# Kernel optimization log

Hardware: AMD Instinct MI355X
Metric: run time of the kernel (lower is better)

The kernel has to match this reference:

```python
import jax, jax.numpy as jnp
import numpy as np

D_MODEL = 1024
N_HEADS = 16
D_FF = 4096
EPS = 1e-5


def setup_inputs() -> dict:
    key = jax.random.key(0)
    ks = jax.random.split(key, 16)
    B, S, D, F = 2, 2048, D_MODEL, D_FF
    s_d = 1.0 / np.sqrt(D)
    s_f = 1.0 / np.sqrt(F)
    return {
        "x": jax.random.normal(ks[0], (B, S, D), dtype=jnp.float32),
        "pad_mask": jnp.ones((B, S), dtype=jnp.int32),
        "ln1_g": jnp.ones((D,), jnp.float32), "ln1_b": jnp.zeros((D,), jnp.float32),
        "ln2_g": jnp.ones((D,), jnp.float32), "ln2_b": jnp.zeros((D,), jnp.float32),
        # weights stored [in, out] (equivalent to torch Linear weight.T)
        "wq": jax.random.normal(ks[1], (D, D), jnp.float32) * s_d,
        "bq": jnp.zeros((D,), jnp.float32),
        "wk": jax.random.normal(ks[2], (D, D), jnp.float32) * s_d,
        "bk": jnp.zeros((D,), jnp.float32),
        "wv": jax.random.normal(ks[3], (D, D), jnp.float32) * s_d,
        "bv": jnp.zeros((D,), jnp.float32),
        "wo": jax.random.normal(ks[4], (D, D), jnp.float32) * s_d,
        "bo": jnp.zeros((D,), jnp.float32),
        "w1": jax.random.normal(ks[5], (D, F), jnp.float32) * s_d,
        "b1": jnp.zeros((F,), jnp.float32),
        "w2": jax.random.normal(ks[6], (F, D), jnp.float32) * s_f,
        "b2": jnp.zeros((D,), jnp.float32),
    }


def _layernorm(x, g, b):
    mu = jnp.mean(x, axis=-1, keepdims=True)
    var = jnp.mean(jnp.square(x - mu), axis=-1, keepdims=True)
    return (x - mu) * jax.lax.rsqrt(var + EPS) * g + b


def reference(x, pad_mask, ln1_g, ln1_b, ln2_g, ln2_b,
              wq, bq, wk, bk, wv, bv, wo, bo, w1, b1, w2, b2):
    B, S, D = x.shape
    H = N_HEADS
    dk = D // H

    # mask: causal [1,1,S,S] * pad [B,1,1,S]
    causal = jnp.tril(jnp.ones((S, S), dtype=jnp.int32))[None, None]
    mask = pad_mask[:, None, None, :] * causal  # [B,1,S,S]

    h = _layernorm(x, ln1_g, ln1_b)
    q = (h @ wq + bq).reshape(B, S, H, dk).transpose(0, 2, 1, 3)
    k = (h @ wk + bk).reshape(B, S, H, dk).transpose(0, 2, 1, 3)
    v = (h @ wv + bv).reshape(B, S, H, dk).transpose(0, 2, 1, 3)

    scores = jnp.einsum('bhqd,bhkd->bhqk', q, k) / np.sqrt(dk)
    scores = jnp.where(mask == 0, -jnp.inf, scores)
    attn = jax.nn.softmax(scores, axis=-1)
    ctx = jnp.einsum('bhqk,bhkd->bhqd', attn, v)
    ctx = ctx.transpose(0, 2, 1, 3).reshape(B, S, D)
    x = x + ctx @ wo + bo

    h2 = _layernorm(x, ln2_g, ln2_b)
    ff = jax.nn.gelu(h2 @ w1 + b1, approximate=False) @ w2 + b2
    return x + ff
```

## Files before the change

kernel.cpp:

```cpp
#include <hip/hip_runtime.h>
#include <math.h>


typedef unsigned short bfu;
typedef unsigned short u16x4 __attribute__((ext_vector_type(4)));
typedef unsigned short u16x8 __attribute__((ext_vector_type(8)));
typedef __bf16         bf16x8 __attribute__((ext_vector_type(8)));
typedef float          f32x4 __attribute__((ext_vector_type(4)));

#define SEQ   2048
#define NTOK  4096
#define DM    1024
#define DKH   64

static __device__ __forceinline__ float bfu2f(bfu u) {
  return __uint_as_float(((unsigned)u) << 16);
}
static __device__ __forceinline__ bfu f2bfu(float f) {
  unsigned u = __float_as_uint(f);
  u += 0x7FFFu + ((u >> 16) & 1u);
  return (bfu)(u >> 16);
}
static __device__ __forceinline__ float ldF(const void* p, size_t i, bool isbf) {
  return isbf ? bfu2f(((const bfu*)p)[i]) : ((const float*)p)[i];
}
static __device__ __forceinline__ bool dt_isbf(const void* dt) {
  return *(const unsigned*)dt == 0x3F803F80u;
}
static __device__ __forceinline__ void g2l16(const void* g, void* l) {
  __builtin_amdgcn_global_load_lds((const __attribute__((address_space(1))) void*)g,
                                   (__attribute__((address_space(3))) void*)l,
                                   16, 0, 0);
}

static __device__ __forceinline__ void tr_tile(const void* in, bfu* out,
                                               int R, int C, int gx, int gy,
                                               bool isbf, bfu t[64][65]) {
  const int tx = threadIdx.x & 63, ty = threadIdx.x >> 6;
#pragma unroll
  for (int i = 0; i < 16; ++i) {
    int rr = i * 4 + ty;
    size_t idx = (size_t)(gy + rr) * C + gx + tx;
    t[rr][tx] = isbf ? ((const bfu*)in)[idx] : f2bfu(((const float*)in)[idx]);
  }
  __syncthreads();
#pragma unroll
  for (int i = 0; i < 16; ++i) {
    int cc = i * 4 + ty;
    out[(size_t)(gx + cc) * R + gy + tx] = t[tx][cc];
  }
}

__global__ __launch_bounds__(256) void prep_k(
    const void* ln1g, const void* ln1b, const void* ln2g, const void* ln2b,
    const void* bq, const void* bk, const void* bv, const void* bo,
    const void* b1, const void* b2,
    const void* wq, const void* wk, const void* wv, const void* wo,
    const void* w1, const void* w2,
    bfu* __restrict__ vecs, bfu* __restrict__ wqkvT, bfu* __restrict__ woT,
    bfu* __restrict__ w1T, bfu* __restrict__ w2T) {
  __shared__ bfu t[64][65];
  const bool isbf = dt_isbf(ln1g);
  const int bid = blockIdx.x, tid = threadIdx.x;
  if (bid < 52) {
    const void* src; int segStart, segDst;
    if      (bid < 4)  { src = ln1g; segStart = 0;  segDst = 0; }
    else if (bid < 8)  { src = ln1b; segStart = 4;  segDst = 1024; }
    else if (bid < 12) { src = ln2g; segStart = 8;  segDst = 2048; }
    else if (bid < 16) { src = ln2b; segStart = 12; segDst = 3072; }
    else if (bid < 20) { src = bq;   segStart = 16; segDst = 4096; }
    else if (bid < 24) { src = bk;   segStart = 20; segDst = 5120; }
    else if (bid < 28) { src = bv;   segStart = 24; segDst = 6144; }
    else if (bid < 32) { src = bo;   segStart = 28; segDst = 7168; }
    else if (bid < 48) { src = b1;   segStart = 32; segDst = 8192; }
    else               { src = b2;   segStart = 48; segDst = 12288; }
    const int off = (bid - segStart) * 256 + tid;
    vecs[segDst + off] = isbf ? ((const bfu*)src)[off]
                              : f2bfu(((const float*)src)[off]);
    return;
  }
  const void* in; bfu* out; int R, C, gx, gy;
  const int j = bid - 52;
  if (j < 1024) {
    const int mat = j >> 8, rem = j & 255;
    in  = (mat == 0) ? wq : (mat == 1) ? wk : (mat == 2) ? wv : wo;
    out = (mat == 0) ? wqkvT : (mat == 1) ? wqkvT + 1048576
        : (mat == 2) ? wqkvT + 2097152 : woT;
    R = 1024; C = 1024; gx = (rem & 15) * 64; gy = (rem >> 4) * 64;
  } else if (j < 2048) {
    const int rem = j - 1024;
    in = w1; out = w1T; R = 1024; C = 4096;
    gx = (rem & 63) * 64; gy = (rem >> 6) * 64;
  } else {
    const int rem = j - 2048;
    in = w2; out = w2T; R = 4096; C = 1024;
    gx = (rem & 15) * 64; gy = (rem >> 4) * 64;
  }
  tr_tile(in, out, R, C, gx, gy, isbf, t);
}

__global__ __launch_bounds__(256) void trw2_k(const void* __restrict__ w2,
                                              bfu* __restrict__ out,
                                              const void* __restrict__ dt) {
  __shared__ bfu t[64][65];
  const bool isbf = dt_isbf(dt);
  const int rem = blockIdx.x;
  tr_tile(w2, out, 4096, 1024, (rem & 15) * 64, (rem >> 4) * 64, isbf, t);
}

template <bool RAW>
__global__ __launch_bounds__(256) void ln_k(const void* __restrict__ xin,
                                            const bfu* __restrict__ g,
                                            const bfu* __restrict__ bb,
                                            bfu* __restrict__ y,
                                            const void* __restrict__ dt) {
  const int t = threadIdx.x;
  const size_t base = (size_t)blockIdx.x * DM;
  const int c0 = t * 4;
  float v[4];
  bool isbf = true;
  if constexpr (RAW) isbf = dt_isbf(dt);
  if (!RAW || isbf) {
    u16x4 u = *(const u16x4*)((const bfu*)xin + base + c0);
#pragma unroll
    for (int i = 0; i < 4; ++i) v[i] = bfu2f(u[i]);
  } else {
    float4 f = *(const float4*)((const float*)xin + base + c0);
    v[0] = f.x; v[1] = f.y; v[2] = f.z; v[3] = f.w;
  }
  float s1 = v[0] + v[1] + v[2] + v[3];
  float s2 = v[0]*v[0] + v[1]*v[1] + v[2]*v[2] + v[3]*v[3];
#pragma unroll
  for (int o = 32; o; o >>= 1) {
    s1 += __shfl_xor(s1, o);
    s2 += __shfl_xor(s2, o);
  }
  __shared__ float r1[4], r2[4];
  const int wid = t >> 6, lane = t & 63;
  if (lane == 0) { r1[wid] = s1; r2[wid] = s2; }
  __syncthreads();
  s1 = r1[0] + r1[1] + r1[2] + r1[3];
  s2 = r2[0] + r2[1] + r2[2] + r2[3];
  const float mu = s1 * (1.0f / DM);
  const float var = s2 * (1.0f / DM) - mu * mu;
  const float rs = rsqrtf(var + 1e-5f);
  u16x4 gv = *(const u16x4*)&g[c0];
  u16x4 bv = *(const u16x4*)&bb[c0];
  u16x4 ov;
#pragma unroll
  for (int i = 0; i < 4; ++i)
    ov[i] = f2bfu((v[i] - mu) * rs * bfu2f(gv[i]) + bfu2f(bv[i]));
  *(u16x4*)&y[base + c0] = ov;
}

template <int EPI>
__global__ __launch_bounds__(256) void gemm_bt(const bfu* __restrict__ A,
                                               const bfu* __restrict__ Bt,
                                               const bfu* __restrict__ bias,
                                               const void* __restrict__ res,
                                               void* __restrict__ C,
                                               int M, int N, int K,
                                               const void* __restrict__ dt) {
  __shared__ __align__(16) bfu Asm[128 * 32];
  __shared__ __align__(16) bfu Bsm[128 * 32];
  const bool isbf = dt_isbf(dt);
  const int tid = threadIdx.x;
  const int m0 = blockIdx.y * 128, n0 = blockIdx.x * 128;
  const int wid = tid >> 6, lane = tid & 63;
  const int wm = (wid >> 1) * 64, wn = (wid & 1) * 64;
  const int quad = lane >> 4, l16 = lane & 15;

  f32x4 acc[4][4] = {};

  const int c0 = tid, c1 = tid + 256;
  const bfu* agp0 = A + (size_t)(m0 + (c0 >> 2)) * K + (c0 & 3) * 8;
  const bfu* agp1 = A + (size_t)(m0 + (c1 >> 2)) * K + (c1 & 3) * 8;
  const bfu* bgp0 = Bt + (size_t)(n0 + (c0 >> 2)) * K + (c0 & 3) * 8;
  const bfu* bgp1 = Bt + (size_t)(n0 + (c1 >> 2)) * K + (c1 & 3) * 8;
  bfu* al0 = Asm + c0 * 8;
  bfu* al1 = Asm + c1 * 8;
  bfu* bl0 = Bsm + c0 * 8;
  bfu* bl1 = Bsm + c1 * 8;

  for (int k0 = 0; k0 < K; k0 += 32) {
    g2l16(agp0 + k0, al0);
    g2l16(agp1 + k0, al1);
    g2l16(bgp0 + k0, bl0);
    g2l16(bgp1 + k0, bl1);
    __syncthreads();

    u16x8 af[4], bfr[4];
#pragma unroll
    for (int i = 0; i < 4; ++i)
      af[i] = *(const u16x8*)&Asm[(wm + i * 16 + l16) * 32 + quad * 8];
#pragma unroll
    for (int i = 0; i < 4; ++i)
      bfr[i] = *(const u16x8*)&Bsm[(wn + i * 16 + l16) * 32 + quad * 8];
#pragma unroll
    for (int mi = 0; mi < 4; ++mi)
#pragma unroll
      for (int ni = 0; ni < 4; ++ni)
        acc[mi][ni] = __builtin_amdgcn_mfma_f32_16x16x32_bf16(
            __builtin_bit_cast(bf16x8, af[mi]),
            __builtin_bit_cast(bf16x8, bfr[ni]), acc[mi][ni], 0, 0, 0);
    __syncthreads();
  }

#pragma unroll
  for (int mi = 0; mi < 4; ++mi) {
#pragma unroll
    for (int ni = 0; ni < 4; ++ni) {
      const int col = n0 + wn + ni * 16 + l16;
      const float bvv = bfu2f(bias[col]);
#pragma unroll
      for (int r = 0; r < 4; ++r) {
        const int row = m0 + wm + mi * 16 + quad * 4 + r;
        const size_t idx = (size_t)row * N + col;
        float v = acc[mi][ni][r] + bvv;
        if constexpr (EPI == 1) {
          v = 0.5f * v * (1.0f + erff(v * 0.70710678118f));
          ((bfu*)C)[idx] = f2bfu(v);
        } else if constexpr (EPI == 2) {
          v += ldF(res, idx, isbf);
          ((bfu*)C)[idx] = f2bfu(v);
        } else if constexpr (EPI == 3) {
          v += bfu2f(((const bfu*)res)[idx]);
          if (isbf) ((bfu*)C)[idx] = f2bfu(v);
          else      ((float*)C)[idx] = v;
        } else {
          ((bfu*)C)[idx] = f2bfu(v);
        }
      }
    }
  }
}

template <int EPI>
__global__ __launch_bounds__(256) void gemm32_bt(const bfu* __restrict__ A,
                                                 const bfu* __restrict__ Bt,
                                                 const bfu* __restrict__ bias,
                                                 const void* __restrict__ res,
                                                 void* __restrict__ C,
                                                 int M, int N, int K,
                                                 const void* __restrict__ dt) {
  __shared__ __align__(16) bfu Asm[2 * 32 * 32];
  __shared__ __align__(16) bfu Bsm[2 * 128 * 32];
  const bool isbf = dt_isbf(dt);
  const int tid = threadIdx.x;
  const int m0 = blockIdx.y * 32, n0 = blockIdx.x * 128;
  const int wid = tid >> 6, lane = tid & 63;
  const int wn = wid * 32;
  const int quad = lane >> 4, l16 = lane & 15;

  f32x4 acc[2][2] = {};

  const int pA = tid >> 7, rA = (tid >> 2) & 31, qA = tid & 3;
  const bfu* agp = A + (size_t)(m0 + rA) * K + pA * 32 + qA * 8;
  bfu* aldst = Asm + tid * 8;
  const bfu* bgp[4]; bfu* bldst[4];
#pragma unroll
  for (int s = 0; s < 4; ++s) {
    const int c = tid + s * 256;
    const int pB = c >> 9, rB = (c >> 2) & 127, qB = c & 3;
    bgp[s] = Bt + (size_t)(n0 + rB) * K + pB * 32 + qB * 8;
    bldst[s] = Bsm + c * 8;
  }

  for (int k0 = 0; k0 < K; k0 += 64) {
    g2l16(agp + k0, aldst);
#pragma unroll
    for (int s = 0; s < 4; ++s) g2l16(bgp[s] + k0, bldst[s]);
    __syncthreads();

    u16x8 af[2][2], bfr[2][2];
#pragma unroll
    for (int kt = 0; kt < 2; ++kt) {
#pragma unroll
      for (int mi = 0; mi < 2; ++mi)
        af[mi][kt] = *(const u16x8*)&Asm[kt * 1024 + (mi * 16 + l16) * 32 + quad * 8];
#pragma unroll
      for (int ni = 0; ni < 2; ++ni)
        bfr[ni][kt] = *(const u16x8*)&Bsm[kt * 4096 + (wn + ni * 16 + l16) * 32 + quad * 8];
    }
#pragma unroll
    for (int kt = 0; kt < 2; ++kt)
#pragma unroll
      for (int mi = 0; mi < 2; ++mi)
#pragma unroll
        for (int ni = 0; ni < 2; ++ni)
          acc[mi][ni] = __builtin_amdgcn_mfma_f32_16x16x32_bf16(
              __builtin_bit_cast(bf16x8, af[mi][kt]),
              __builtin_bit_cast(bf16x8, bfr[ni][kt]), acc[mi][ni], 0, 0, 0);
    __syncthreads();
  }

#pragma unroll
  for (int mi = 0; mi < 2; ++mi) {
#pragma unroll
    for (int ni = 0; ni < 2; ++ni) {
      const int col = n0 + wn + ni * 16 + l16;
      const float bvv = bfu2f(bias[col]);
#pragma unroll
      for (int r = 0; r < 4; ++r) {
        const int row = m0 + mi * 16 + quad * 4 + r;
        const size_t idx = (size_t)row * N + col;
        float v = acc[mi][ni][r] + bvv;
        if constexpr (EPI == 1) {
          v = 0.5f * v * (1.0f + erff(v * 0.70710678118f));
          ((bfu*)C)[idx] = f2bfu(v);
        } else if constexpr (EPI == 2) {
          v += ldF(res, idx, isbf);
          ((bfu*)C)[idx] = f2bfu(v);
        } else if constexpr (EPI == 3) {
          v += bfu2f(((const bfu*)res)[idx]);
          if (isbf) ((bfu*)C)[idx] = f2bfu(v);
          else      ((float*)C)[idx] = v;
        } else {
          ((bfu*)C)[idx] = f2bfu(v);
        }
      }
    }
  }
}

#define NEG_BIG (-1e30f)
#define KSTR 72

__global__ __launch_bounds__(256) void attn_flash(const bfu* __restrict__ qkv,
                                                  const int* __restrict__ pad,
                                                  bfu* __restrict__ ctx) {
  __shared__ __align__(16) bfu Kb[64 * KSTR];
  __shared__ __align__(16) bfu VT[64 * KSTR];
  __shared__ __align__(16) bfu Pb[4][16 * KSTR];

  const int tid = threadIdx.x;
  const int wid = tid >> 6, lane = tid & 63;
  const int quad = lane >> 4, l16 = lane & 15;
  const int bh = blockIdx.x;
  const int b = bh >> 4, h = bh & 15;
  const int yq = blockIdx.y;
  const int qt = (yq < 8) ? yq : (yq < 16) ? 23 - yq
               : (yq < 24) ? yq : 55 - yq;
  const int q0 = qt * 64;

  const bfu* qptr = qkv + (size_t)(b * SEQ + q0 + wid * 16 + l16) * 3072 + h * 64 + quad * 8;
  u16x8 qfr[2];
#pragma unroll
  for (int kt = 0; kt < 2; ++kt) {
    u16x8 qr = *(const u16x8*)(qptr + kt * 32);
#pragma unroll
    for (int j = 0; j < 8; ++j) qr[j] = f2bfu(bfu2f(qr[j]) * 0.125f);
    qfr[kt] = qr;
  }

  f32x4 Ofr[4] = {};
  float mrow[4], lrow[4];
#pragma unroll
  for (int r = 0; r < 4; ++r) { mrow[r] = NEG_BIG; lrow[r] = 0.0f; }

  const bfu* kvbase = qkv + (size_t)(b * SEQ) * 3072 + h * 64;
  const int* pb = pad + b * SEQ;
  const int qrow_base = q0 + wid * 16 + quad * 4;

  const int kkey0 = tid >> 3,          kpc0 = tid & 7;
  const int kkey1 = (tid + 256) >> 3,  kpc1 = (tid + 256) & 7;
  const int vkey = tid & 63, dblk = tid >> 6;

  u16x8 kreg0, kreg1, vreg0, vreg1;
  kreg0 = *(const u16x8*)(kvbase + (size_t)kkey0 * 3072 + 1024 + kpc0 * 8);
  kreg1 = *(const u16x8*)(kvbase + (size_t)kkey1 * 3072 + 1024 + kpc1 * 8);
  vreg0 = *(const u16x8*)(kvbase + (size_t)vkey * 3072 + 2048 + dblk * 16);
  vreg1 = *(const u16x8*)(kvbase + (size_t)vkey * 3072 + 2048 + dblk * 16 + 8);

  const int ntiles = qt + 1;
  for (int t = 0; t < ntiles; ++t) {
    const int k0 = t * 64;
    __syncthreads();

    *(u16x8*)&Kb[kkey0 * KSTR + kpc0 * 8] = kreg0;
    *(u16x8*)&Kb[kkey1 * KSTR + kpc1 * 8] = kreg1;
#pragma unroll
    for (int j = 0; j < 8; ++j) VT[(dblk * 16 + j) * KSTR + vkey] = vreg0[j];
#pragma unroll
    for (int j = 0; j < 8; ++j) VT[(dblk * 16 + 8 + j) * KSTR + vkey] = vreg1[j];
    __syncthreads();

    if (t + 1 < ntiles) {
      const int kn = k0 + 64;
      kreg0 = *(const u16x8*)(kvbase + (size_t)(kn + kkey0) * 3072 + 1024 + kpc0 * 8);
      kreg1 = *(const u16x8*)(kvbase + (size_t)(kn + kkey1) * 3072 + 1024 + kpc1 * 8);
      vreg0 = *(const u16x8*)(kvbase + (size_t)(kn + vkey) * 3072 + 2048 + dblk * 16);
      vreg1 = *(const u16x8*)(kvbase + (size_t)(kn + vkey) * 3072 + 2048 + dblk * 16 + 8);
    }

    f32x4 S[4] = {};
#pragma unroll
    for (int nt = 0; nt < 4; ++nt)
#pragma unroll
      for (int kt = 0; kt < 2; ++kt) {
        u16x8 bf = *(const u16x8*)&Kb[(nt * 16 + l16) * KSTR + kt * 32 + quad * 8];
        S[nt] = __builtin_amdgcn_mfma_f32_16x16x32_bf16(
            __builtin_bit_cast(bf16x8, qfr[kt]),
            __builtin_bit_cast(bf16x8, bf), S[nt], 0, 0, 0);
      }

    const bool edge = (t == qt);
    float p[4][4];
    float cmax[4] = {NEG_BIG, NEG_BIG, NEG_BIG, NEG_BIG};
#pragma unroll
    for (int nt = 0; nt < 4; ++nt) {
      const int key = k0 + nt * 16 + l16;
      const bool ok = (pb[key] != 0);
#pragma unroll
      for (int r = 0; r < 4; ++r) {
        float s = (ok && (!edge || key <= qrow_base + r)) ? S[nt][r] : NEG_BIG;
        p[nt][r] = s;
        cmax[r] = fmaxf(cmax[r], s);
      }
    }
#pragma unroll
    for (int off = 1; off < 16; off <<= 1)
#pragma unroll
      for (int r = 0; r < 4; ++r)
        cmax[r] = fmaxf(cmax[r], __shfl_xor(cmax[r], off));
    float alpha[4];
#pragma unroll
    for (int r = 0; r < 4; ++r) {
      const float mn = fmaxf(mrow[r], cmax[r]);
      alpha[r] = __expf(mrow[r] - mn);
      mrow[r] = mn;
    }
    float psum[4] = {0, 0, 0, 0};
#pragma unroll
    for (int nt = 0; nt < 4; ++nt)
#pragma unroll
      for (int r = 0; r < 4; ++r) {
        p[nt][r] = __expf(p[nt][r] - mrow[r]);
        psum[r] += p[nt][r];
      }
#pragma unroll
    for (int off = 1; off < 16; off <<= 1)
#pragma unroll
      for (int r = 0; r < 4; ++r) psum[r] += __shfl_xor(psum[r], off);
#pragma unroll
    for (int r = 0; r < 4; ++r) lrow[r] = lrow[r] * alpha[r] + psum[r];
#pragma unroll
    for (int n = 0; n < 4; ++n)
#pragma unroll
      for (int r = 0; r < 4; ++r) Ofr[n][r] *= alpha[r];

#pragma unroll
    for (int nt = 0; nt < 4; ++nt)
#pragma unroll
      for (int r = 0; r < 4; ++r)
        Pb[wid][(quad * 4 + r) * KSTR + nt * 16 + l16] = f2bfu(p[nt][r]);

#pragma unroll
    for (int at = 0; at < 2; ++at) {
      u16x8 af = *(const u16x8*)&Pb[wid][l16 * KSTR + at * 32 + quad * 8];
#pragma unroll
      for (int n = 0; n < 4; ++n) {
        u16x8 bf = *(const u16x8*)&VT[(n * 16 + l16) * KSTR + at * 32 + quad * 8];
        Ofr[n] = __builtin_amdgcn_mfma_f32_16x16x32_bf16(
            __builtin_bit_cast(bf16x8, af),
            __builtin_bit_cast(bf16x8, bf), Ofr[n], 0, 0, 0);
      }
    }
  }

  float inv[4];
#pragma unroll
  for (int r = 0; r < 4; ++r) inv[r] = 1.0f / lrow[r];
#pragma unroll
  for (int n = 0; n < 4; ++n)
#pragma unroll
    for (int r = 0; r < 4; ++r)
      ctx[(size_t)(b * SEQ + qrow_base + r) * DM + h * 64 + n * 16 + l16] =
          f2bfu(Ofr[n][r] * inv[r]);
}

extern "C" void kernel_launch(void* const* d_in, const int* in_sizes, int n_in,
                              void* d_out, int out_size, void* d_ws, size_t ws_size,
                              hipStream_t stream) {
  (void)in_sizes; (void)n_in; (void)out_size;
  const void* x    = d_in[0];
  const int*  pad  = (const int*)d_in[1];
  const void* ln1g = d_in[2];
  const void* ln1b = d_in[3];
  const void* ln2g = d_in[4];
  const void* ln2b = d_in[5];
  const void* wq   = d_in[6];
  const void* bq   = d_in[7];
  const void* wk   = d_in[8];
  const void* bk   = d_in[9];
  const void* wv   = d_in[10];
  const void* bv   = d_in[11];
  const void* wo   = d_in[12];
  const void* bo   = d_in[13];
  const void* w1   = d_in[14];
  const void* b1   = d_in[15];
  const void* w2   = d_in[16];
  const void* b2   = d_in[17];

  const bool flat = ws_size >= (size_t)(37765120 + 1024) * 2;
  bfu* base  = (bfu*)d_ws;
  bfu* vecs  = base;
  bfu* wqkvT = vecs  + 16384;
  bfu* woT   = wqkvT + 3145728;
  bfu* w1T   = woT   + 1048576;
  bfu* w2Tf  = w1T   + 4194304;
  bfu* h     = w2Tf  + (flat ? 4194304 : 0);
  bfu* qkv   = h     + 4194304;
  bfu* ctx   = qkv   + 12582912;
  bfu* x1    = ctx   + 4194304;
  bfu* ffh   = qkv;
  bfu* w2T   = flat ? w2Tf : h;

  const dim3 blk(256);
  bfu* lg1 = vecs;        bfu* lb1 = vecs + 1024;
  bfu* lg2 = vecs + 2048; bfu* lb2 = vecs + 3072;
  bfu* bqkv = vecs + 4096;
  bfu* boc  = vecs + 7168;
  bfu* b1c  = vecs + 8192;
  bfu* b2c  = vecs + 12288;

  prep_k<<<dim3(flat ? 3124 : 2100), blk, 0, stream>>>(
      ln1g, ln1b, ln2g, ln2b, bq, bk, bv, bo, b1, b2,
      wq, wk, wv, wo, w1, w2, vecs, wqkvT, woT, w1T, w2T);

  ln_k<true><<<dim3(NTOK), blk, 0, stream>>>(x, lg1, lb1, h, ln1g);
  gemm_bt<0><<<dim3(24, 32), blk, 0, stream>>>(h, wqkvT, bqkv, nullptr,
                                               qkv, NTOK, 3072, 1024, ln1g);
  attn_flash<<<dim3(32, 32), blk, 0, stream>>>(qkv, pad, ctx);
  gemm32_bt<2><<<dim3(8, 128), blk, 0, stream>>>(ctx, woT, boc, x, x1,
                                                 NTOK, 1024, 1024, ln1g);
  ln_k<false><<<dim3(NTOK), blk, 0, stream>>>(x1, lg2, lb2, h, ln1g);
  gemm_bt<1><<<dim3(32, 32), blk, 0, stream>>>(h, w1T, b1c, nullptr, ffh,
                                               NTOK, 4096, 1024, ln1g);
  if (!flat) trw2_k<<<dim3(1024), blk, 0, stream>>>(w2, w2T, ln1g);
  gemm32_bt<3><<<dim3(8, 128), blk, 0, stream>>>(ffh, w2T, b2c, x1, d_out,
                                                 NTOK, 1024, 4096, ln1g);
}
```

Before: 452.4 us.

## Pre-transpose V into global buffer and read K/V fragments directly from global memory

Adds a separate kernel that transposes the V slice of the QKV buffer into a per-head [d][seq] layout stored in the free h workspace. The attention kernel then drops its shared-memory K and V staging, the two block barriers per tile and the register prefetch, and loads MFMA B-fragments for K and V straight from global memory. The aim is to remove LDS traffic, the scalar transposing stores into LDS and the barrier stalls. In exchange it adds a kernel launch plus an extra write and read of V, and each wave fetches K/V separately through cache, with no software prefetch to hide global latency.

Result: slower. 494.6 us (+9.3%).

```diff
diff --git a/kernel.cpp b/kernel.cpp
--- a/kernel.cpp
+++ b/kernel.cpp
@@ -108,6 +108,25 @@
   tr_tile(w2, out, 4096, 1024, (rem & 15) * 64, (rem >> 4) * 64, isbf, t);
 }
 
+__global__ __launch_bounds__(256) void vtr_k(const bfu* __restrict__ qkv,
+                                             bfu* __restrict__ vT) {
+  __shared__ bfu t[64][65];
+  const int bh = blockIdx.x, st = blockIdx.y;
+  const int b = bh >> 4, h = bh & 15;
+  const int tx = threadIdx.x & 63, ty = threadIdx.x >> 6;
+#pragma unroll
+  for (int i = 0; i < 16; ++i) {
+    const int s = i * 4 + ty;
+    t[s][tx] = qkv[(size_t)(b * SEQ + st * 64 + s) * 3072 + 2048 + h * 64 + tx];
+  }
+  __syncthreads();
+#pragma unroll
+  for (int i = 0; i < 16; ++i) {
+    const int d = i * 4 + ty;
+    vT[(size_t)bh * (64 * SEQ) + (size_t)d * SEQ + st * 64 + tx] = t[tx][d];
+  }
+}
+
 template <bool RAW>
 __global__ __launch_bounds__(256) void ln_k(const void* __restrict__ xin,
                                             const bfu* __restrict__ g,
@@ -327,10 +346,9 @@
 #define KSTR 72
 
 __global__ __launch_bounds__(256) void attn_flash(const bfu* __restrict__ qkv,
+                                                  const bfu* __restrict__ vT,
                                                   const int* __restrict__ pad,
                                                   bfu* __restrict__ ctx) {
-  __shared__ __align__(16) bfu Kb[64 * KSTR];
-  __shared__ __align__(16) bfu VT[64 * KSTR];
   __shared__ __align__(16) bfu Pb[4][16 * KSTR];
 
   const int tid = threadIdx.x;
@@ -358,51 +376,27 @@
 #pragma unroll
   for (int r = 0; r < 4; ++r) { mrow[r] = NEG_BIG; lrow[r] = 0.0f; }
 
-  const bfu* kvbase = qkv + (size_t)(b * SEQ) * 3072 + h * 64;
+  const bfu* kfb = qkv + (size_t)(b * SEQ + l16) * 3072 + 1024 + h * 64 + quad * 8;
+  const bfu* vfb = vT + (size_t)bh * (64 * SEQ) + (size_t)l16 * SEQ + quad * 8;
   const int* pb = pad + b * SEQ;
   const int qrow_base = q0 + wid * 16 + quad * 4;
-
-  const int kkey0 = tid >> 3,          kpc0 = tid & 7;
-  const int kkey1 = (tid + 256) >> 3,  kpc1 = (tid + 256) & 7;
-  const int vkey = tid & 63, dblk = tid >> 6;
-
-  u16x8 kreg0, kreg1, vreg0, vreg1;
-  kreg0 = *(const u16x8*)(kvbase + (size_t)kkey0 * 3072 + 1024 + kpc0 * 8);
-  kreg1 = *(const u16x8*)(kvbase + (size_t)kkey1 * 3072 + 1024 + kpc1 * 8);
-  vreg0 = *(const u16x8*)(kvbase + (size_t)vkey * 3072 + 2048 + dblk * 16);
-  vreg1 = *(const u16x8*)(kvbase + (size_t)vkey * 3072 + 2048 + dblk * 16 + 8);
 
   const int ntiles = qt + 1;
   for (int t = 0; t < ntiles; ++t) {
     const int k0 = t * 64;
-    __syncthreads();
-
-    *(u16x8*)&Kb[kkey0 * KSTR + kpc0 * 8] = kreg0;
-    *(u16x8*)&Kb[kkey1 * KSTR + kpc1 * 8] = kreg1;
-#pragma unroll
-    for (int j = 0; j < 8; ++j) VT[(dblk * 16 + j) * KSTR + vkey] = vreg0[j];
-#pragma unroll
-    for (int j = 0; j < 8; ++j) VT[(dblk * 16 + 8 + j) * KSTR + vkey] = vreg1[j];
-    __syncthreads();
-
-    if (t + 1 < ntiles) {
-      const int kn = k0 + 64;
-      kreg0 = *(const u16x8*)(kvbase + (size_t)(kn + kkey0) * 3072 + 1024 + kpc0 * 8);
-      kreg1 = *(const u16x8*)(kvbase + (size_t)(kn + kkey1) * 3072 + 1024 + kpc1 * 8);
-      vreg0 = *(const u16x8*)(kvbase + (size_t)(kn + vkey) * 3072 + 2048 + dblk * 16);
-      vreg1 = *(const u16x8*)(kvbase + (size_t)(kn + vkey) * 3072 + 2048 + dblk * 16 + 8);
-    }
 
     f32x4 S[4] = {};
 #pragma unroll
-    for (int nt = 0; nt < 4; ++nt)
+    for (int nt = 0; nt < 4; ++nt) {
+      const bfu* kp = kfb + (size_t)(k0 + nt * 16) * 3072;
 #pragma unroll
       for (int kt = 0; kt < 2; ++kt) {
-        u16x8 bf = *(const u16x8*)&Kb[(nt * 16 + l16) * KSTR + kt * 32 + quad * 8];
+        u16x8 bf = *(const u16x8*)(kp + kt * 32);
         S[nt] = __builtin_amdgcn_mfma_f32_16x16x32_bf16(
             __builtin_bit_cast(bf16x8, qfr[kt]),
             __builtin_bit_cast(bf16x8, bf), S[nt], 0, 0, 0);
       }
+    }
 
     const bool edge = (t == qt);
     float p[4][4];
@@ -460,7 +454,7 @@
       u16x8 af = *(const u16x8*)&Pb[wid][l16 * KSTR + at * 32 + quad * 8];
 #pragma unroll
       for (int n = 0; n < 4; ++n) {
-        u16x8 bf = *(const u16x8*)&VT[(n * 16 + l16) * KSTR + at * 32 + quad * 8];
+        u16x8 bf = *(const u16x8*)(vfb + (size_t)(n * 16) * SEQ + k0 + at * 32);
         Ofr[n] = __builtin_amdgcn_mfma_f32_16x16x32_bf16(
             __builtin_bit_cast(bf16x8, af),
             __builtin_bit_cast(bf16x8, bf), Ofr[n], 0, 0, 0);
@@ -515,6 +509,7 @@
   bfu* x1    = ctx   + 4194304;
   bfu* ffh   = qkv;
   bfu* w2T   = flat ? w2Tf : h;
+  bfu* vT    = h;
 
   const dim3 blk(256);
   bfu* lg1 = vecs;        bfu* lb1 = vecs + 1024;
@@ -531,7 +526,8 @@
   ln_k<true><<<dim3(NTOK), blk, 0, stream>>>(x, lg1, lb1, h, ln1g);
   gemm_bt<0><<<dim3(24, 32), blk, 0, stream>>>(h, wqkvT, bqkv, nullptr,
                                                qkv, NTOK, 3072, 1024, ln1g);
-  attn_flash<<<dim3(32, 32), blk, 0, stream>>>(qkv, pad, ctx);
+  vtr_k<<<dim3(32, 32), blk, 0, stream>>>(qkv, vT);
+  attn_flash<<<dim3(32, 32), blk, 0, stream>>>(qkv, vT, pad, ctx);
   gemm32_bt<2><<<dim3(8, 128), blk, 0, stream>>>(ctx, woT, boc, x, x1,
                                                  NTOK, 1024, 1024, ln1g);
   ln_k<false><<<dim3(NTOK), blk, 0, stream>>>(x1, lg2, lb2, h, ln1g);
```
